# Kernel optimization log

Hardware: AMD Instinct MI355X
Metric: run time of the kernel (lower is better)

## Reference

```python
import jax, jax.numpy as jnp
import numpy as np

B, S, D, NQ, NC, MC, K = 64, 200, 128, 50000, 1000, 4, 10
N = NQ + NC  # total graph nodes (concepts first, then questions, matching torch concat order)


def setup_inputs() -> dict:
    key = jax.random.key(0)
    ks = jax.random.split(key, 32)
    f = lambda i, shape: jax.random.normal(ks[i], shape, dtype=jnp.float32) * 0.02
    return {
        "emb_q": f(0, (NQ, D)), "emb_c": f(1, (NC, D)), "emb_r": f(2, (2, D)),
        "Wih1": f(3, (3 * D, 2 * D)), "Whh1": f(4, (3 * D, D)), "bih1": f(5, (3 * D,)), "bhh1": f(6, (3 * D,)),
        "Wih2": f(7, (3 * D, D)), "Whh2": f(8, (3 * D, D)), "bih2": f(9, (3 * D,)), "bhh2": f(10, (3 * D,)),
        "Wg1": f(11, (D, D)), "Wg2": f(12, (D, D)), "Wg3": f(13, (D, D)),
        "Wagg": f(14, (D, D)), "bagg": f(15, (D,)),
        "Wq": f(16, (D, D)), "bq": f(17, (D,)),
        "Wk": f(18, (D, D)), "bk": f(19, (D,)),
        "Ww": f(20, (1, 2 * D)), "bw": f(21, (1,)),
        "question_seq": jax.random.randint(ks[22], (B, S), 0, NQ),
        "correct_seq": jax.random.randint(ks[23], (B, S), 0, 2),
        "mask_seq": jnp.ones((B, S), dtype=jnp.int32),
        "q_table": jax.random.randint(ks[24], (NQ, MC), 0, NC),
    }


def _gru(x, h, Wih, Whh, bih, bhh):
    gi = x @ Wih.T + bih
    gh = h @ Whh.T + bhh
    i_r, i_z, i_n = jnp.split(gi, 3, axis=-1)
    h_r, h_z, h_n = jnp.split(gh, 3, axis=-1)
    r = jax.nn.sigmoid(i_r + h_r)
    z = jax.nn.sigmoid(i_z + h_z)
    n = jnp.tanh(i_n + r * h_n)
    return (1.0 - z) * n + z * h


def _sage_mean(x, src, dst, W):
    # SAGEConv4GIKT (eval): out = lin_r(mean_agg_over_neighbors + x), lin_r has no bias.
    agg = jax.ops.segment_sum(x[dst], src, num_segments=N)
    cnt = jax.ops.segment_sum(jnp.ones((src.shape[0], 1), x.dtype), src, num_segments=N)
    agg = agg / jnp.maximum(cnt, 1.0)
    return (agg + x) @ W.T


def reference(emb_q, emb_c, emb_r, Wih1, Whh1, bih1, bhh1, Wih2, Whh2, bih2, bhh2,
              Wg1, Wg2, Wg3, Wagg, bagg, Wq, bq, Wk, bk, Ww, bw,
              question_seq, correct_seq, mask_seq, q_table):
    # ---- GNN propagation over the full question-concept bipartite graph ----
    x = jnp.concatenate([emb_c, emb_q], axis=0)  # [N, D], concepts first
    q_glob = jnp.repeat(jnp.arange(NQ, dtype=q_table.dtype) + NC, MC)  # question global ids
    c_glob = q_table.reshape(-1)                                       # concept global ids
    x = _sage_mean(x, q_glob, c_glob, Wg1)  # q2c: aggregate at questions from concepts
    x = _sage_mean(x, c_glob, q_glob, Wg2)  # c2q: aggregate at concepts from questions
    x = _sage_mean(x, q_glob, c_glob, Wg3)  # q2c again
    x = jnp.tanh(x @ Wagg.T + bagg)

    tgrid = jnp.arange(S)

    def step(carry, inp):
        h1, h2, keyhist, statehist = carry
        t, q_t, r_t, m_t, q_next = inp
        m = (m_t != 0)[:, None]
        e_q = jnp.where(m, x[q_t + NC], emb_q[q_t])  # GNN emb where masked-in, raw emb otherwise
        e_r = emb_r[r_t]
        h1 = _gru(jnp.concatenate([e_q, e_r], axis=1), h1, Wih1, Whh1, bih1, bhh1)
        h2 = _gru(h1, h2, Wih2, Whh2, bih2, bhh2)
        statehist = statehist.at[:, t].set(h2)
        keyhist = keyhist.at[:, t].set(h2 @ Wk.T + bk)
        # queries: next question emb + its concept embs -> [B, MC+1, D]
        qc = jnp.concatenate([emb_q[q_next][:, None, :], emb_c[q_table[q_next]]], axis=1)
        aq = qc @ Wq.T + bq
        scores = jnp.einsum('bid,bjd->bij', aq, keyhist)  # [B, MC+1, S]
        scores = jnp.where((tgrid <= t)[None, None, :], scores, -1e9)
        flat = scores.reshape(B, -1)
        vals, idx = jax.lax.top_k(flat, K)  # top-k (query, state) pairs
        alpha = jax.nn.softmax(vals, axis=-1)
        i_idx = idx // S
        j_idx = idx % S
        q_sel = jnp.take_along_axis(qc, i_idx[:, :, None], axis=1)        # [B, K, D]
        s_sel = jnp.take_along_axis(statehist, j_idx[:, :, None], axis=1)  # [B, K, D]
        f = jax.nn.sigmoid(jnp.concatenate([q_sel, s_sel], axis=-1) @ Ww.T + bw)[..., 0]
        y = jnp.sum(alpha * f, axis=-1)  # [B]
        return (h1, h2, keyhist, statehist), y

    h0 = jnp.zeros((B, D), jnp.float32)
    carry = (h0, h0, jnp.zeros((B, S, D), jnp.float32), jnp.zeros((B, S, D), jnp.float32))
    xs = (jnp.arange(S - 1), question_seq[:, :-1].T, correct_seq[:, :-1].T,
          mask_seq[:, :-1].T, question_seq[:, 1:].T)
    _, ys = jax.lax.scan(step, carry, xs)
    y_hat = jnp.concatenate([jnp.zeros((B, 1), jnp.float32), ys.T], axis=1)  # predictions for t=1..S-1
    return y_hat
```

## Files before the change

### kernel.cpp

```cpp
#include <hip/hip_runtime.h>
#include <math.h>

#define Bz 64
#define Sz 200
#define Dz 128
#define NQz 50000
#define NCz 1000
#define MCz 4
#define Kz 10
#define Tz 199
#define NSz (Bz*Tz)
#define NEz (NQz*MCz)
#define KTpad 256

__global__ void k_count(const int* __restrict__ qt, int* __restrict__ cnt) {
    int e = blockIdx.x*256 + threadIdx.x;
    if (e < NEz) atomicAdd(&cnt[qt[e]], 1);
}

__global__ void k_offs(const int* __restrict__ cnt, int* __restrict__ offs) {
    __shared__ int s[1024];
    int tid = threadIdx.x;
    s[tid] = (tid < NCz) ? cnt[tid] : 0;
    __syncthreads();
    for (int off = 1; off < 1024; off <<= 1) {
        int add = (tid >= off) ? s[tid - off] : 0;
        __syncthreads();
        s[tid] += add;
        __syncthreads();
    }
    if (tid < NCz) offs[tid + 1] = s[tid];
    if (tid == 0) offs[0] = 0;
}

__global__ void k_fill(const int* __restrict__ qt, const int* __restrict__ offs,
                       int* __restrict__ fill, int* __restrict__ edge_q) {
    int e = blockIdx.x*256 + threadIdx.x;
    if (e < NEz) {
        int c = qt[e];
        int pos = atomicAdd(&fill[c], 1);
        edge_q[offs[c] + pos] = e >> 2;
    }
}

__global__ void k_m2(const int* __restrict__ qt, const int* __restrict__ offs,
                     const int* __restrict__ edge_q,
                     const float* __restrict__ emb_q, const float* __restrict__ emb_c,
                     float* __restrict__ m2) {
    int c = blockIdx.x;
    int g = threadIdx.x >> 7;
    int d = threadIdx.x & 127;
    int e0 = offs[c], e1 = offs[c+1];
    float acc = 0.f;
    for (int e = e0 + g; e < e1; e += 4) {
        int q = edge_q[e];
        const int* t4 = qt + q*4;
        int c0 = t4[0], c1 = t4[1], c2 = t4[2], c3 = t4[3];
        acc += emb_q[q*128 + d]
             + 0.25f*(emb_c[c0*128+d] + emb_c[c1*128+d] + emb_c[c2*128+d] + emb_c[c3*128+d]);
    }
    __shared__ float ps[4][128];
    ps[g][d] = acc;
    __syncthreads();
    if (g == 0) {
        float tot = ps[0][d] + ps[1][d] + ps[2][d] + ps[3][d];
        float cn = (float)(e1 - e0);
        m2[c*128 + d] = tot / fmaxf(cn, 1.0f);
    }
}

template<bool TR>
__global__ void k_mm128(const float* __restrict__ X, const float* __restrict__ Y,
                        float* __restrict__ out) {
    int r = blockIdx.x, c = threadIdx.x;
    float acc = 0.f;
    for (int e = 0; e < 128; ++e) acc += X[r*128 + e] * Y[e*128 + c];
    if (TR) out[c*128 + r] = acc;
    else    out[r*128 + c] = acc;
}

__global__ void k_gr(const float* __restrict__ emb_r, const float* __restrict__ Wih1,
                     const float* __restrict__ bih1, float* __restrict__ gr) {
    int rt = threadIdx.x / 384, r = threadIdx.x % 384;
    float acc = bih1[r];
    for (int e = 0; e < 128; ++e) acc += emb_r[rt*128 + e] * Wih1[r*256 + 128 + e];
    gr[rt*384 + r] = acc;
}

__global__ void k_bkq(const float* __restrict__ Wq, const float* __restrict__ Wk,
                      const float* __restrict__ bq, const float* __restrict__ bk,
                      const float* __restrict__ Ww, const float* __restrict__ bw,
                      float* __restrict__ Bkq, float* __restrict__ biaskq) {
    int r = blockIdx.x, d = threadIdx.x;
    if (r < 128) {
        float acc = 0.f;
        for (int n = 0; n < 128; ++n) acc += Wq[n*128 + r] * Wk[n*128 + d];
        Bkq[r*128 + d] = acc;
        if (d == 0) {
            float b0 = 0.f;
            for (int n = 0; n < 128; ++n) b0 += Wq[n*128 + r] * bk[n];
            biaskq[r] = b0;
        }
    } else if (r == 128) {
        float acc = 0.f;
        for (int n = 0; n < 128; ++n) acc += bq[n] * Wk[n*128 + d];
        Bkq[128*128 + d] = acc;
        if (d == 0) {
            float c0 = 0.f;
            for (int n = 0; n < 128; ++n) c0 += bq[n] * bk[n];
            biaskq[128] = c0;
        }
    } else {
        Bkq[129*128 + d] = Ww[128 + d];
        if (d == 0) biaskq[129] = bw[0];
    }
}

__global__ void k_eq(const float* __restrict__ Mt_g, const float* __restrict__ bagg,
                     const float* __restrict__ emb_q, const float* __restrict__ emb_c,
                     const float* __restrict__ m2, const int* __restrict__ qseq,
                     const int* __restrict__ mseq, const int* __restrict__ qt,
                     float* __restrict__ eq) {
    __shared__ float Mt[128*128];
    __shared__ float ub[2][128];
    int tid = threadIdx.x;
    for (int i = tid; i < 128*128/4; i += 256)
        ((float4*)Mt)[i] = ((const float4*)Mt_g)[i];
    __syncthreads();
    int g = tid >> 7, d = tid & 127;
    for (int it = 0; it < 8; ++it) {
        int slot = blockIdx.x*16 + it*2 + g;
        int b = slot / Tz, t = slot % Tz;
        int q = qseq[b*Sz + t];
        int msk = mseq[b*Sz + t];
        if (msk) {
            const int* t4 = qt + q*4;
            int c0 = t4[0], c1 = t4[1], c2 = t4[2], c3 = t4[3];
            ub[g][d] = emb_q[q*128 + d]
                     + 0.5f *(emb_c[c0*128+d] + emb_c[c1*128+d] + emb_c[c2*128+d] + emb_c[c3*128+d])
                     + 0.25f*(m2[c0*128+d]  + m2[c1*128+d]  + m2[c2*128+d]  + m2[c3*128+d]);
        }
        __syncthreads();
        if (msk) {
            float acc = bagg[d];
            const float* urow = ub[g];
            for (int e = 0; e < 128; ++e) acc += Mt[e*128 + d] * urow[e];
            eq[slot*128 + d] = tanhf(acc);
        } else {
            eq[slot*128 + d] = emb_q[q*128 + d];
        }
        __syncthreads();
    }
}

__device__ __forceinline__ float bf_lo(unsigned u){ return __uint_as_float(u << 16); }
__device__ __forceinline__ float bf_hi(unsigned u){ return __uint_as_float(u & 0xffff0000u); }
__device__ __forceinline__ unsigned f2bf(float x){
    unsigned u = __float_as_uint(x);
    return (u + 0x7fffu + ((u >> 16) & 1u)) >> 16;
}
__device__ __forceinline__ unsigned pk2(float a, float b){
    return f2bf(a) | (f2bf(b) << 16);
}
__device__ __forceinline__ float rcpf(float x){ return __builtin_amdgcn_rcpf(x); }
__device__ __forceinline__ float sigm(float x){ return rcpf(1.f + __expf(-x)); }
__device__ __forceinline__ float tanh_fast(float x){
    float e = __expf(2.f*x);
    return 1.f - 2.f*rcpf(e + 1.f);
}

#if __has_builtin(__builtin_amdgcn_fdot2_f32_bf16)
typedef __attribute__((ext_vector_type(2))) short short2v;
__device__ __forceinline__ float bdot2(unsigned w, unsigned h, float acc) {
    return __builtin_amdgcn_fdot2_f32_bf16(__builtin_bit_cast(short2v, w),
                                           __builtin_bit_cast(short2v, h), acc, false);
}
#else
__device__ __forceinline__ float bdot2(unsigned w, unsigned h, float acc) {
    return acc + bf_lo(w)*bf_lo(h) + bf_hi(w)*bf_hi(h);
}
#endif

typedef __attribute__((ext_vector_type(2))) float v2f;
__device__ __forceinline__ void pkfma_lo(v2f &acc, v2f k, v2f q) {
    asm("v_pk_fma_f32 %0, %1, %2, %0 op_sel_hi:[1,0,1]"
        : "+v"(acc) : "v"(k), "v"(q));
}
__device__ __forceinline__ void pkfma_hi(v2f &acc, v2f k, v2f q) {
    asm("v_pk_fma_f32 %0, %1, %2, %0 op_sel:[0,1,0] op_sel_hi:[1,1,1]"
        : "+v"(acc) : "v"(k), "v"(q));
}

template<int MODE, int DOT2>
__global__ void k_gemm(const float* __restrict__ A, const float* __restrict__ Bm,
                       int ldb, int nB, float* __restrict__ C, int ldc,
                       const float* __restrict__ bias, const float* __restrict__ gr,
                       const int* __restrict__ cseq) {
    __shared__ int rtb[64];
    int tx = threadIdx.x, ty = threadIdx.y;
    int tid = ty*16 + tx;
    int m0 = blockIdx.x * 64;
    int n0 = blockIdx.y * 64;
    if (MODE == 1 && tid < 64) {
        int s = m0 + tid;
        int b = s / Tz, t = s % Tz;
        rtb[tid] = cseq[b*Sz + t];
    }
    float acc[4][4];
    #pragma unroll
    for (int i = 0; i < 4; ++i)
        #pragma unroll
        for (int j = 0; j < 4; ++j) acc[i][j] = 0.f;

    if (DOT2) {
        __shared__ unsigned As[64][17];
        __shared__ unsigned Bs[64][17];
        for (int kc = 0; kc < 128; kc += 32) {
            #pragma unroll
            for (int l = 0; l < 2; ++l) {
                int v = tid*2 + l;
                int row = v >> 3, c4 = (v & 7) << 2;
                int p0 = (kc + c4) >> 1 & 15;
                float4 av = *(const float4*)(A + (size_t)(m0+row)*128 + kc + c4);
                As[row][p0]   = pk2(av.x, av.y);
                As[row][p0+1] = pk2(av.z, av.w);
                int nrow = n0 + row;
                float4 bv = make_float4(0.f, 0.f, 0.f, 0.f);
                if (nrow < nB) bv = *(const float4*)(Bm + (size_t)nrow*ldb + kc + c4);
                Bs[row][p0]   = pk2(bv.x, bv.y);
                Bs[row][p0+1] = pk2(bv.z, bv.w);
            }
            __syncthreads();
            #pragma unroll 4
            for (int kp = 0; kp < 16; ++kp) {
                unsigned av[4], bv[4];
                #pragma unroll
                for (int i = 0; i < 4; ++i) av[i] = As[ty*4+i][kp];
                #pragma unroll
                for (int j = 0; j < 4; ++j) bv[j] = Bs[tx*4+j][kp];
                #pragma unroll
                for (int i = 0; i < 4; ++i)
                    #pragma unroll
                    for (int j = 0; j < 4; ++j) acc[i][j] = bdot2(av[i], bv[j], acc[i][j]);
            }
            __syncthreads();
        }
    } else {
        __shared__ float Asf[64][33];
        __shared__ float Bsf[64][33];
        for (int kc = 0; kc < 128; kc += 32) {
            #pragma unroll
            for (int l = 0; l < 2; ++l) {
                int v = tid*2 + l;
                int row = v >> 3, c4 = (v & 7) << 2;
                float4 av = *(const float4*)(A + (size_t)(m0+row)*128 + kc + c4);
                Asf[row][c4+0] = av.x; Asf[row][c4+1] = av.y; Asf[row][c4+2] = av.z; Asf[row][c4+3] = av.w;
                int nrow = n0 + row;
                float4 bv = make_float4(0.f, 0.f, 0.f, 0.f);
                if (nrow < nB) bv = *(const float4*)(Bm + (size_t)nrow*ldb + kc + c4);
                Bsf[row][c4+0] = bv.x; Bsf[row][c4+1] = bv.y; Bsf[row][c4+2] = bv.z; Bsf[row][c4+3] = bv.w;
            }
            __syncthreads();
            #pragma unroll 8
            for (int k = 0; k < 32; ++k) {
                float av[4], bv[4];
                #pragma unroll
                for (int i = 0; i < 4; ++i) av[i] = Asf[ty*4+i][k];
                #pragma unroll
                for (int j = 0; j < 4; ++j) bv[j] = Bsf[tx*4+j][k];
                #pragma unroll
                for (int i = 0; i < 4; ++i)
                    #pragma unroll
                    for (int j = 0; j < 4; ++j) acc[i][j] += av[i]*bv[j];
            }
            __syncthreads();
        }
    }
    #pragma unroll
    for (int i = 0; i < 4; ++i) {
        int s = m0 + ty*4 + i;
        if (MODE == 2) {
            int bb = s / Tz, tt = s - ((int)(s / Tz))*Tz;
            #pragma unroll
            for (int j = 0; j < 4; ++j) {
                int col = n0 + tx*4 + j;
                if (col < nB)
                    C[((size_t)bb*132 + col)*KTpad + tt] = acc[i][j] + bias[col];
            }
        } else {
            #pragma unroll
            for (int j = 0; j < 4; ++j) {
                int col = n0 + tx*4 + j;
                if (col < nB) {
                    float v = acc[i][j];
                    if (MODE == 0) v += bias[col];
                    else           v += gr[rtb[ty*4+i]*384 + col];
                    C[(size_t)s*ldc + col] = v;
                }
            }
        }
    }
}

__global__ void __launch_bounds__(512, 1)
k_scan(const float* __restrict__ gi, const float* __restrict__ Whh,
       const float* __restrict__ bhh, float* __restrict__ hout) {
    int b = blockIdx.x, tid = threadIdx.x;
    int wid = tid >> 6, lane = tid & 63;
    int u  = wid*16 + (lane & 15);
    int qh = lane >> 4;

    unsigned wr[16], wz[16], wn[16];
    {
        const float4* r4 = (const float4*)(Whh + (size_t)u*128       + qh*32);
        const float4* z4 = (const float4*)(Whh + (size_t)(u+128)*128 + qh*32);
        const float4* n4 = (const float4*)(Whh + (size_t)(u+256)*128 + qh*32);
        #pragma unroll
        for (int k = 0; k < 8; ++k) {
            float4 a = r4[k]; wr[2*k] = pk2(a.x, a.y); wr[2*k+1] = pk2(a.z, a.w);
            float4 c = z4[k]; wz[2*k] = pk2(c.x, c.y); wz[2*k+1] = pk2(c.z, c.w);
            float4 d = n4[k]; wn[2*k] = pk2(d.x, d.y); wn[2*k+1] = pk2(d.z, d.w);
        }
    }
    float br = bhh[u], bz = bhh[u+128], bn = bhh[u+256];

    __shared__ unsigned hb[2][64];
    if (tid < 64) { hb[0][tid] = 0u; hb[1][tid] = 0u; }
    float hold = 0.f;

    const float* gbase = gi + (size_t)(b*Tz)*384;
    float gc0 = gbase[u], gc1 = gbase[u+128], gc2 = gbase[u+256];
    float ga0 = gbase[384+u], ga1 = gbase[384+u+128], ga2 = gbase[384+u+256];
    __syncthreads();

    for (int t = 0; t < Tz; ++t) {
        float gm0 = 0.f, gm1 = 0.f, gm2 = 0.f;
        if (t + 2 < Tz) {
            const float* gp = gbase + (size_t)(t+2)*384;
            gm0 = gp[u]; gm1 = gp[u+128]; gm2 = gp[u+256];
        }
        const unsigned* hc = hb[t & 1];
        const uint4* hv = (const uint4*)(hc + qh*16);
        uint4 h0 = hv[0], h1 = hv[1], h2 = hv[2], h3 = hv[3];
        float ar, az, an;
        {
            float p0=0.f, p1=0.f;
            p0 = bdot2(wr[0],  h0.x, p0); p1 = bdot2(wr[1],  h0.y, p1);
            p0 = bdot2(wr[2],  h0.z, p0); p1 = bdot2(wr[3],  h0.w, p1);
            p0 = bdot2(wr[4],  h1.x, p0); p1 = bdot2(wr[5],  h1.y, p1);
            p0 = bdot2(wr[6],  h1.z, p0); p1 = bdot2(wr[7],  h1.w, p1);
            p0 = bdot2(wr[8],  h2.x, p0); p1 = bdot2(wr[9],  h2.y, p1);
            p0 = bdot2(wr[10], h2.z, p0); p1 = bdot2(wr[11], h2.w, p1);
            p0 = bdot2(wr[12], h3.x, p0); p1 = bdot2(wr[13], h3.y, p1);
            p0 = bdot2(wr[14], h3.z, p0); p1 = bdot2(wr[15], h3.w, p1);
            ar = p0 + p1;
        }
        {
            float p0=0.f, p1=0.f;
            p0 = bdot2(wz[0],  h0.x, p0); p1 = bdot2(wz[1],  h0.y, p1);
            p0 = bdot2(wz[2],  h0.z, p0); p1 = bdot2(wz[3],  h0.w, p1);
            p0 = bdot2(wz[4],  h1.x, p0); p1 = bdot2(wz[5],  h1.y, p1);
            p0 = bdot2(wz[6],  h1.z, p0); p1 = bdot2(wz[7],  h1.w, p1);
            p0 = bdot2(wz[8],  h2.x, p0); p1 = bdot2(wz[9],  h2.y, p1);
            p0 = bdot2(wz[10], h2.z, p0); p1 = bdot2(wz[11], h2.w, p1);
            p0 = bdot2(wz[12], h3.x, p0); p1 = bdot2(wz[13], h3.y, p1);
            p0 = bdot2(wz[14], h3.z, p0); p1 = bdot2(wz[15], h3.w, p1);
            az = p0 + p1;
        }
        {
            float p0=0.f, p1=0.f;
            p0 = bdot2(wn[0],  h0.x, p0); p1 = bdot2(wn[1],  h0.y, p1);
            p0 = bdot2(wn[2],  h0.z, p0); p1 = bdot2(wn[3],  h0.w, p1);
            p0 = bdot2(wn[4],  h1.x, p0); p1 = bdot2(wn[5],  h1.y, p1);
            p0 = bdot2(wn[6],  h1.z, p0); p1 = bdot2(wn[7],  h1.w, p1);
            p0 = bdot2(wn[8],  h2.x, p0); p1 = bdot2(wn[9],  h2.y, p1);
            p0 = bdot2(wn[10], h2.z, p0); p1 = bdot2(wn[11], h2.w, p1);
            p0 = bdot2(wn[12], h3.x, p0); p1 = bdot2(wn[13], h3.y, p1);
            p0 = bdot2(wn[14], h3.z, p0); p1 = bdot2(wn[15], h3.w, p1);
            an = p0 + p1;
        }
        ar += __shfl_xor(ar, 16); ar += __shfl_xor(ar, 32);
        az += __shfl_xor(az, 16); az += __shfl_xor(az, 32);
        an += __shfl_xor(an, 16); an += __shfl_xor(an, 32);
        float rr = sigm(gc0 + br + ar);
        float zz = sigm(gc1 + bz + az);
        float nn = tanh_fast(gc2 + rr*(bn + an));
        float hnew = (1.f - zz)*nn + zz*hold;
        hold = hnew;
        if (qh == 0) {
            ((unsigned short*)hb[(t & 1) ^ 1])[u] = (unsigned short)f2bf(hnew);
            hout[(size_t)(b*Tz + t)*128 + u] = hnew;
        }
        gc0 = ga0; gc1 = ga1; gc2 = ga2;
        ga0 = gm0; ga1 = gm1; ga2 = gm2;
        __syncthreads();
    }
}

__global__ void __launch_bounds__(256, 1)
k_attn(const float* __restrict__ kqt, const int* __restrict__ qseq,
       const int* __restrict__ qt, const float* __restrict__ emb_q,
       const float* __restrict__ emb_c, const float* __restrict__ Ww,
       float* __restrict__ out) {
    int wid  = threadIdx.x >> 6;
    int lane = threadIdx.x & 63;
    int b = blockIdx.y;
    int t = blockIdx.x*4 + wid;
    if (t > Tz - 1) t = Tz - 1;

    __shared__ float qc[4][5][128];
    __shared__ float gqs[4][5];
    int qn = qseq[b*Sz + t + 1];
    for (int idx = lane; idx < 5*128; idx += 64) {
        int i = idx / 128, d = idx & 127;
        const float* src = (i == 0) ? (emb_q + (size_t)qn*128)
                                    : (emb_c + (size_t)qt[qn*4 + (i-1)]*128);
        qc[wid][i][d] = src[d];
    }
    __syncthreads();
    {
        float w0 = Ww[lane], w1 = Ww[lane + 64];
        #pragma unroll
        for (int i = 0; i < 5; ++i) {
            float p = qc[wid][i][lane]*w0 + qc[wid][i][lane+64]*w1;
            #pragma unroll
            for (int off = 32; off >= 1; off >>= 1) p += __shfl_xor(p, off);
            if (lane == 0) gqs[wid][i] = p;
        }
    }
    __syncthreads();

    const float* base = kqt + (size_t)b*(132*KTpad);

    v2f accA[5], accB[5];
    #pragma unroll
    for (int i = 0; i < 5; ++i) { accA[i] = (v2f){0.f,0.f}; accB[i] = (v2f){0.f,0.f}; }

    #pragma unroll 2
    for (int c = 0; c < 32; ++c) {
        float4 k0 = ((const float4*)(base + (size_t)(4*c+0)*KTpad))[lane];
        float4 k1 = ((const float4*)(base + (size_t)(4*c+1)*KTpad))[lane];
        float4 k2 = ((const float4*)(base + (size_t)(4*c+2)*KTpad))[lane];
        float4 k3 = ((const float4*)(base + (size_t)(4*c+3)*KTpad))[lane];
        v2f k0a = {k0.x,k0.y}, k0b = {k0.z,k0.w};
        v2f k1a = {k1.x,k1.y}, k1b = {k1.z,k1.w};
        v2f k2a = {k2.x,k2.y}, k2b = {k2.z,k2.w};
        v2f k3a = {k3.x,k3.y}, k3b = {k3.z,k3.w};
        #pragma unroll
        for (int i = 0; i < 5; ++i) {
            float4 q = ((const float4*)qc[wid][i])[c];
            v2f qa = {q.x,q.y}, qb = {q.z,q.w};
            pkfma_lo(accA[i], k0a, qa); pkfma_lo(accB[i], k0b, qa);
            pkfma_hi(accA[i], k1a, qa); pkfma_hi(accB[i], k1b, qa);
            pkfma_lo(accA[i], k2a, qb); pkfma_lo(accB[i], k2b, qb);
            pkfma_hi(accA[i], k3a, qb); pkfma_hi(accB[i], k3b, qb);
        }
    }

    const float NEG = -3.402823466e38f;
    float sv[10]; int si[10];
    #pragma unroll
    for (int k = 0; k < 10; ++k) { sv[k] = NEG; si[k] = 0x7FFFFFFF; }

    auto ins = [&](float cv, int ci) {
        if (cv > sv[9] || (cv == sv[9] && ci < si[9])) {
            #pragma unroll
            for (int k = 0; k < 10; ++k) {
                bool bet = (cv > sv[k]) || (cv == sv[k] && ci < si[k]);
                float tv = sv[k]; int ti = si[k];
                if (bet) { sv[k] = cv; si[k] = ci; cv = tv; ci = ti; }
            }
        }
    };
    {
        float4 kb4 = ((const float4*)(base + 128*KTpad))[lane];
        float kbv[4] = {kb4.x, kb4.y, kb4.z, kb4.w};
        #pragma unroll
        for (int jj = 0; jj < 4; ++jj) {
            int j = 4*lane + jj;
            if (j <= t) {
                #pragma unroll
                for (int i = 0; i < 5; ++i) {
                    float a = (jj == 0) ? accA[i].x : (jj == 1) ? accA[i].y
                            : (jj == 2) ? accB[i].x : accB[i].y;
                    ins(a + kbv[jj], i*Sz + j);
                }
            }
        }
    }

    float vmax = 0.f, myv = 0.f; int myidx = 0x7FFFFFFF;
    #pragma unroll
    for (int rnd = 0; rnd < 10; ++rnd) {
        float v = sv[0]; int idx = si[0];
        #pragma unroll
        for (int off = 32; off >= 1; off >>= 1) {
            float ov = __shfl_xor(v, off);
            int   oi = __shfl_xor(idx, off);
            if (ov > v || (ov == v && oi < idx)) { v = ov; idx = oi; }
        }
        if (rnd == 0) vmax = v;
        if (lane == rnd) { myv = v; myidx = idx; }
        if (si[0] == idx) {
            #pragma unroll
            for (int k = 0; k < 9; ++k) { sv[k] = sv[k+1]; si[k] = si[k+1]; }
            sv[9] = NEG; si[9] = 0x7FFFFFFF;
        }
    }

    float num = 0.f, den = 0.f;
    if (lane < 10 && myidx != 0x7FFFFFFF) {
        float a = __expf(myv - vmax);
        int ik = myidx / Sz, jk = myidx % Sz;
        float gsj = base[129*KTpad + jk];
        float f = sigm(gqs[wid][ik] + gsj);
        num = a*f; den = a;
    }
    #pragma unroll
    for (int off = 32; off >= 1; off >>= 1) {
        num += __shfl_xor(num, off);
        den += __shfl_xor(den, off);
    }
    if (lane == 0) out[b*Sz + t + 1] = num/den;
}

static inline size_t alup(size_t x) { return (x + 255) & ~(size_t)255; }

extern "C" void kernel_launch(void* const* d_in, const int* in_sizes, int n_in,
                              void* d_out, int out_size, void* d_ws, size_t ws_size,
                              hipStream_t stream) {
    (void)in_sizes; (void)n_in; (void)ws_size;
    const float* emb_q = (const float*)d_in[0];
    const float* emb_c = (const float*)d_in[1];
    const float* emb_r = (const float*)d_in[2];
    const float* Wih1  = (const float*)d_in[3];
    const float* Whh1  = (const float*)d_in[4];
    const float* bih1  = (const float*)d_in[5];
    const float* bhh1  = (const float*)d_in[6];
    const float* Wih2  = (const float*)d_in[7];
    const float* Whh2  = (const float*)d_in[8];
    const float* bih2  = (const float*)d_in[9];
    const float* bhh2  = (const float*)d_in[10];
    const float* Wg1   = (const float*)d_in[11];
    const float* Wg2   = (const float*)d_in[12];
    const float* Wg3   = (const float*)d_in[13];
    const float* Wagg  = (const float*)d_in[14];
    const float* bagg  = (const float*)d_in[15];
    const float* Wq    = (const float*)d_in[16];
    const float* bq    = (const float*)d_in[17];
    const float* Wk    = (const float*)d_in[18];
    const float* bk    = (const float*)d_in[19];
    const float* Ww    = (const float*)d_in[20];
    const float* bw    = (const float*)d_in[21];
    const int* qseq    = (const int*)d_in[22];
    const int* cseq    = (const int*)d_in[23];
    const int* mseq    = (const int*)d_in[24];
    const int* qtab    = (const int*)d_in[25];
    float* out = (float*)d_out;

    char* p = (char*)d_ws;
    auto alloc = [&](size_t bytes) { char* r = p; p += alup(bytes); return r; };
    int*   cnt    = (int*)  alloc(4096);
    int*   fill   = (int*)  alloc(4096);
    int*   offs   = (int*)  alloc(1001*4);
    int*   edge_q = (int*)  alloc((size_t)NEz*4);
    float* m2     = (float*)alloc((size_t)NCz*128*4);
    float* T1     = (float*)alloc(128*128*4);
    float* T2     = (float*)alloc(128*128*4);
    float* Mt     = (float*)alloc(128*128*4);
    float* gr     = (float*)alloc(2*384*4);
    float* Bkq    = (float*)alloc(132*128*4);
    float* biaskq = (float*)alloc(132*4);
    float* eq     = (float*)alloc((size_t)NSz*128*4);
    float* gi1    = (float*)alloc((size_t)NSz*384*4);
    float* stateh = (float*)alloc((size_t)NSz*128*4);
    float* kqt    = (float*)alloc((size_t)Bz*132*KTpad*4);
    float* h1all = eq;
    float* gi2   = gi1;

    hipMemsetAsync(cnt, 0, 8192, stream);
    hipMemsetAsync(d_out, 0, (size_t)out_size*4, stream);

    k_count<<<(NEz+255)/256, 256, 0, stream>>>(qtab, cnt);
    k_offs <<<1, 1024, 0, stream>>>(cnt, offs);
    k_fill <<<(NEz+255)/256, 256, 0, stream>>>(qtab, offs, fill, edge_q);
    k_m2   <<<NCz, 512, 0, stream>>>(qtab, offs, edge_q, emb_q, emb_c, m2);

    k_mm128<false><<<128, 128, 0, stream>>>(Wg2, Wg1, T1);
    k_mm128<false><<<128, 128, 0, stream>>>(Wg3, T1, T2);
    k_mm128<true> <<<128, 128, 0, stream>>>(Wagg, T2, Mt);
    k_gr  <<<1, 768, 0, stream>>>(emb_r, Wih1, bih1, gr);
    k_bkq <<<130, 128, 0, stream>>>(Wq, Wk, bq, bk, Ww, bw, Bkq, biaskq);

    k_eq  <<<NSz/16, 256, 0, stream>>>(Mt, bagg, emb_q, emb_c, m2, qseq, mseq, qtab, eq);

    k_gemm<1,1><<<dim3(NSz/64, 6), dim3(16,16), 0, stream>>>(eq, Wih1, 256, 384,
                                                             gi1, 384, nullptr, gr, cseq);
    k_scan<<<Bz, 512, 0, stream>>>(gi1, Whh1, bhh1, h1all);
    k_gemm<0,1><<<dim3(NSz/64, 6), dim3(16,16), 0, stream>>>(h1all, Wih2, 128, 384,
                                                             gi2, 384, bih2, nullptr, nullptr);
    k_scan<<<Bz, 512, 0, stream>>>(gi2, Whh2, bhh2, stateh);

    k_gemm<2,0><<<dim3(NSz/64, 3), dim3(16,16), 0, stream>>>(stateh, Bkq, 128, 132,
                                                             kqt, 0, biaskq, nullptr, nullptr);
    k_attn<<<dim3((Tz+3)/4, Bz), 256, 0, stream>>>(kqt, qseq, qtab, emb_q, emb_c, Ww, out);
}
```

Baseline: 695.3 us.

## Stage GRU input projections in double-buffered shared-memory chunks

The recurrent GRU kernel used to load each timestep's input-gate values from global memory two steps ahead, holding them in registers. It now prefetches chunks of 8 timesteps cooperatively into double-buffered shared memory, staging the next chunk in registers while the current chunk is processed. The aim is to take global-load latency off the serial per-step critical path and make the loads coalesced. In exchange it uses more shared memory, adds an extra barrier per chunk, and holds six staging registers across the inner loop.

```diff
diff --git a/kernel.cpp b/kernel.cpp
--- a/kernel.cpp
+++ b/kernel.cpp
@@ -12,6 +12,7 @@
 #define NSz (Bz*Tz)
 #define NEz (NQz*MCz)
 #define KTpad 256
+#define CHz 8
 
 __global__ void k_count(const int* __restrict__ qt, int* __restrict__ cnt) {
     int e = blockIdx.x*256 + threadIdx.x;
@@ -325,75 +326,105 @@
     float br = bhh[u], bz = bhh[u+128], bn = bhh[u+256];
 
     __shared__ unsigned hb[2][64];
+    __shared__ float gis[2][CHz][384];
     if (tid < 64) { hb[0][tid] = 0u; hb[1][tid] = 0u; }
     float hold = 0.f;
 
     const float* gbase = gi + (size_t)(b*Tz)*384;
-    float gc0 = gbase[u], gc1 = gbase[u+128], gc2 = gbase[u+256];
-    float ga0 = gbase[384+u], ga1 = gbase[384+u+128], ga2 = gbase[384+u+256];
+    {
+        #pragma unroll
+        for (int k = 0; k < 6; ++k) {
+            int f = tid + k*512;
+            int s = f / 384, d = f - s*384;
+            int tt = s; if (tt > Tz-1) tt = Tz-1;
+            gis[0][s][d] = gbase[(size_t)tt*384 + d];
+        }
+    }
     __syncthreads();
 
-    for (int t = 0; t < Tz; ++t) {
-        float gm0 = 0.f, gm1 = 0.f, gm2 = 0.f;
-        if (t + 2 < Tz) {
-            const float* gp = gbase + (size_t)(t+2)*384;
-            gm0 = gp[u]; gm1 = gp[u+128]; gm2 = gp[u+256];
-        }
-        const unsigned* hc = hb[t & 1];
-        const uint4* hv = (const uint4*)(hc + qh*16);
-        uint4 h0 = hv[0], h1 = hv[1], h2 = hv[2], h3 = hv[3];
-        float ar, az, an;
-        {
-            float p0=0.f, p1=0.f;
-            p0 = bdot2(wr[0],  h0.x, p0); p1 = bdot2(wr[1],  h0.y, p1);
-            p0 = bdot2(wr[2],  h0.z, p0); p1 = bdot2(wr[3],  h0.w, p1);
-            p0 = bdot2(wr[4],  h1.x, p0); p1 = bdot2(wr[5],  h1.y, p1);
-            p0 = bdot2(wr[6],  h1.z, p0); p1 = bdot2(wr[7],  h1.w, p1);
-            p0 = bdot2(wr[8],  h2.x, p0); p1 = bdot2(wr[9],  h2.y, p1);
-            p0 = bdot2(wr[10], h2.z, p0); p1 = bdot2(wr[11], h2.w, p1);
-            p0 = bdot2(wr[12], h3.x, p0); p1 = bdot2(wr[13], h3.y, p1);
-            p0 = bdot2(wr[14], h3.z, p0); p1 = bdot2(wr[15], h3.w, p1);
-            ar = p0 + p1;
-        }
-        {
-            float p0=0.f, p1=0.f;
-            p0 = bdot2(wz[0],  h0.x, p0); p1 = bdot2(wz[1],  h0.y, p1);
-            p0 = bdot2(wz[2],  h0.z, p0); p1 = bdot2(wz[3],  h0.w, p1);
-            p0 = bdot2(wz[4],  h1.x, p0); p1 = bdot2(wz[5],  h1.y, p1);
-            p0 = bdot2(wz[6],  h1.z, p0); p1 = bdot2(wz[7],  h1.w, p1);
-            p0 = bdot2(wz[8],  h2.x, p0); p1 = bdot2(wz[9],  h2.y, p1);
-            p0 = bdot2(wz[10], h2.z, p0); p1 = bdot2(wz[11], h2.w, p1);
-            p0 = bdot2(wz[12], h3.x, p0); p1 = bdot2(wz[13], h3.y, p1);
-            p0 = bdot2(wz[14], h3.z, p0); p1 = bdot2(wz[15], h3.w, p1);
-            az = p0 + p1;
-        }
-        {
-            float p0=0.f, p1=0.f;
-            p0 = bdot2(wn[0],  h0.x, p0); p1 = bdot2(wn[1],  h0.y, p1);
-            p0 = bdot2(wn[2],  h0.z, p0); p1 = bdot2(wn[3],  h0.w, p1);
-            p0 = bdot2(wn[4],  h1.x, p0); p1 = bdot2(wn[5],  h1.y, p1);
-            p0 = bdot2(wn[6],  h1.z, p0); p1 = bdot2(wn[7],  h1.w, p1);
-            p0 = bdot2(wn[8],  h2.x, p0); p1 = bdot2(wn[9],  h2.y, p1);
-            p0 = bdot2(wn[10], h2.z, p0); p1 = bdot2(wn[11], h2.w, p1);
-            p0 = bdot2(wn[12], h3.x, p0); p1 = bdot2(wn[13], h3.y, p1);
-            p0 = bdot2(wn[14], h3.z, p0); p1 = bdot2(wn[15], h3.w, p1);
-            an = p0 + p1;
-        }
-        ar += __shfl_xor(ar, 16); ar += __shfl_xor(ar, 32);
-        az += __shfl_xor(az, 16); az += __shfl_xor(az, 32);
-        an += __shfl_xor(an, 16); an += __shfl_xor(an, 32);
-        float rr = sigm(gc0 + br + ar);
-        float zz = sigm(gc1 + bz + az);
-        float nn = tanh_fast(gc2 + rr*(bn + an));
-        float hnew = (1.f - zz)*nn + zz*hold;
-        hold = hnew;
-        if (qh == 0) {
-            ((unsigned short*)hb[(t & 1) ^ 1])[u] = (unsigned short)f2bf(hnew);
-            hout[(size_t)(b*Tz + t)*128 + u] = hnew;
-        }
-        gc0 = ga0; gc1 = ga1; gc2 = ga2;
-        ga0 = gm0; ga1 = gm1; ga2 = gm2;
-        __syncthreads();
+    const int nch = (Tz + CHz - 1) / CHz;
+    for (int c = 0; c < nch; ++c) {
+        float stg0=0.f, stg1=0.f, stg2=0.f, stg3=0.f, stg4=0.f, stg5=0.f;
+        if (c + 1 < nch) {
+            #pragma unroll
+            for (int k = 0; k < 6; ++k) {
+                int f = tid + k*512;
+                int s = f / 384, d = f - s*384;
+                int tt = (c+1)*CHz + s; if (tt > Tz-1) tt = Tz-1;
+                float v = gbase[(size_t)tt*384 + d];
+                if (k==0) stg0=v; else if (k==1) stg1=v; else if (k==2) stg2=v;
+                else if (k==3) stg3=v; else if (k==4) stg4=v; else stg5=v;
+            }
+        }
+        int smax = Tz - c*CHz; if (smax > CHz) smax = CHz;
+        for (int s = 0; s < smax; ++s) {
+            int t = c*CHz + s;
+            const float* grow = gis[c & 1][s];
+            float gc0 = grow[u], gc1 = grow[u+128], gc2 = grow[u+256];
+            const unsigned* hc = hb[t & 1];
+            const uint4* hv = (const uint4*)(hc + qh*16);
+            uint4 h0 = hv[0], h1 = hv[1], h2 = hv[2], h3 = hv[3];
+            float ar, az, an;
+            {
+                float p0=0.f, p1=0.f;
+                p0 = bdot2(wr[0],  h0.x, p0); p1 = bdot2(wr[1],  h0.y, p1);
+                p0 = bdot2(wr[2],  h0.z, p0); p1 = bdot2(wr[3],  h0.w, p1);
+                p0 = bdot2(wr[4],  h1.x, p0); p1 = bdot2(wr[5],  h1.y, p1);
+                p0 = bdot2(wr[6],  h1.z, p0); p1 = bdot2(wr[7],  h1.w, p1);
+                p0 = bdot2(wr[8],  h2.x, p0); p1 = bdot2(wr[9],  h2.y, p1);
+                p0 = bdot2(wr[10], h2.z, p0); p1 = bdot2(wr[11], h2.w, p1);
+                p0 = bdot2(wr[12], h3.x, p0); p1 = bdot2(wr[13], h3.y, p1);
+                p0 = bdot2(wr[14], h3.z, p0); p1 = bdot2(wr[15], h3.w, p1);
+                ar = p0 + p1;
+            }
+            {
+                float p0=0.f, p1=0.f;
+                p0 = bdot2(wz[0],  h0.x, p0); p1 = bdot2(wz[1],  h0.y, p1);
+                p0 = bdot2(wz[2],  h0.z, p0); p1 = bdot2(wz[3],  h0.w, p1);
+                p0 = bdot2(wz[4],  h1.x, p0); p1 = bdot2(wz[5],  h1.y, p1);
+                p0 = bdot2(wz[6],  h1.z, p0); p1 = bdot2(wz[7],  h1.w, p1);
+                p0 = bdot2(wz[8],  h2.x, p0); p1 = bdot2(wz[9],  h2.y, p1);
+                p0 = bdot2(wz[10], h2.z, p0); p1 = bdot2(wz[11], h2.w, p1);
+                p0 = bdot2(wz[12], h3.x, p0); p1 = bdot2(wz[13], h3.y, p1);
+                p0 = bdot2(wz[14], h3.z, p0); p1 = bdot2(wz[15], h3.w, p1);
+                az = p0 + p1;
+            }
+            {
+                float p0=0.f, p1=0.f;
+                p0 = bdot2(wn[0],  h0.x, p0); p1 = bdot2(wn[1],  h0.y, p1);
+                p0 = bdot2(wn[2],  h0.z, p0); p1 = bdot2(wn[3],  h0.w, p1);
+                p0 = bdot2(wn[4],  h1.x, p0); p1 = bdot2(wn[5],  h1.y, p1);
+                p0 = bdot2(wn[6],  h1.z, p0); p1 = bdot2(wn[7],  h1.w, p1);
+                p0 = bdot2(wn[8],  h2.x, p0); p1 = bdot2(wn[9],  h2.y, p1);
+                p0 = bdot2(wn[10], h2.z, p0); p1 = bdot2(wn[11], h2.w, p1);
+                p0 = bdot2(wn[12], h3.x, p0); p1 = bdot2(wn[13], h3.y, p1);
+                p0 = bdot2(wn[14], h3.z, p0); p1 = bdot2(wn[15], h3.w, p1);
+                an = p0 + p1;
+            }
+            ar += __shfl_xor(ar, 16); ar += __shfl_xor(ar, 32);
+            az += __shfl_xor(az, 16); az += __shfl_xor(az, 32);
+            an += __shfl_xor(an, 16); an += __shfl_xor(an, 32);
+            float rr = sigm(gc0 + br + ar);
+            float zz = sigm(gc1 + bz + az);
+            float nn = tanh_fast(gc2 + rr*(bn + an));
+            float hnew = (1.f - zz)*nn + zz*hold;
+            hold = hnew;
+            if (qh == 0) {
+                ((unsigned short*)hb[(t & 1) ^ 1])[u] = (unsigned short)f2bf(hnew);
+                hout[(size_t)(b*Tz + t)*128 + u] = hnew;
+            }
+            __syncthreads();
+        }
+        if (c + 1 < nch) {
+            float stg[6] = {stg0, stg1, stg2, stg3, stg4, stg5};
+            #pragma unroll
+            for (int k = 0; k < 6; ++k) {
+                int f = tid + k*512;
+                int s = f / 384, d = f - s*384;
+                gis[(c+1) & 1][s][d] = stg[k];
+            }
+            __syncthreads();
+        }
     }
 }
 
```

Result: faster. 668.8 us (-3.8%).
